# Kernel tuning notes

Hardware: AMD Instinct MI355X
Metric: run time of the kernel (lower is better)

Reference implementation:

```python
import jax, jax.numpy as jnp
import numpy as np
import math

D = 256
NH = 4
MULT = 128
N = MULT * D // NH  # 8192
N_LAYER = 6
VOCAB = 256
THETA = 2 ** 16
EPS = 1e-5


def get_freqs(n):
    ar = jnp.arange(n, dtype=jnp.float32)
    q = jnp.floor(ar / 2.0) * 2.0  # quantize in pairs
    return 1.0 / (THETA ** (q / n)) / (2.0 * math.pi)


def layer_norm(x):
    m = jnp.mean(x, axis=-1, keepdims=True)
    v = jnp.var(x, axis=-1, keepdims=True)
    return (x - m) / jnp.sqrt(v + EPS)


def rope_apply(v, cos, sin):
    # interleaved rotation: v_rot = stack((-v[odd], v[even])) interleaved back
    v_rot = jnp.stack([-v[..., 1::2], v[..., ::2]], axis=-1).reshape(v.shape)
    return v * cos + v_rot * sin


def setup_inputs() -> dict:
    key = jax.random.key(0)
    ks = jax.random.split(key, 6)
    idx = jax.random.randint(ks[0], (1, 1024), 0, VOCAB)
    embed = jax.random.normal(ks[1], (VOCAB, D), dtype=jnp.float32) * 0.02
    encoder = jax.random.normal(ks[2], (NH, D, N), dtype=jnp.float32) * 0.02
    encoder_v = jax.random.normal(ks[3], (NH, D, N), dtype=jnp.float32) * 0.02
    decoder = jax.random.normal(ks[4], (NH * N, D), dtype=jnp.float32) * 0.02
    lm_head = jax.random.normal(ks[5], (D, VOCAB), dtype=jnp.float32) * 0.02
    return {"idx": idx, "embed": embed, "encoder": encoder,
            "encoder_v": encoder_v, "decoder": decoder, "lm_head": lm_head}


def reference(idx, embed, encoder, encoder_v, decoder, lm_head):
    B, T = idx.shape
    x = layer_norm(embed[idx])  # (B, T, D)

    freqs = get_freqs(N)  # (N,)
    phases = (jnp.arange(T, dtype=jnp.float32)[:, None] * freqs[None, :]) % 1.0
    phases = phases * (2.0 * math.pi)
    cos = jnp.cos(phases)[None, None]  # (1,1,T,N)
    sin = jnp.sin(phases)[None, None]

    causal = jnp.tril(jnp.ones((T, T), dtype=jnp.float32), k=-1)  # strict lower

    for _ in range(N_LAYER):
        # x_sparse: (B, nh, T, N)
        x_sparse = jax.nn.relu(jnp.einsum('btd,hdn->bhtn', x, encoder))
        QR = rope_apply(x_sparse, cos, sin)
        # raw (no-softmax) strictly-causal attention, V = x broadcast over heads
        scores = jnp.einsum('bhtn,bhsn->bhts', QR, QR) * causal
        yKV = layer_norm(jnp.einsum('bhts,bsd->bhtd', scores, x))
        y_sparse = jax.nn.relu(jnp.einsum('bhtd,hdn->bhtn', yKV, encoder_v))
        xy = x_sparse * y_sparse  # (B, nh, T, N)
        # head-major flatten then project back to D
        yMLP = xy.transpose(0, 2, 1, 3).reshape(B, T, NH * N) @ decoder
        y = layer_norm(yMLP)
        x = layer_norm(x + y)

    logits = x @ lm_head  # (B, T, VOCAB)
    return logits
```

## Files before the change

### kernel.cpp

```cpp
#include <hip/hip_runtime.h>
#include <math.h>


typedef __bf16 bf16;
typedef bf16  bf16x8 __attribute__((ext_vector_type(8)));
typedef float f32x4  __attribute__((ext_vector_type(4)));

#define BM 128
#define BN 128
#define BK 32
#define SW 32

typedef __attribute__((address_space(3))) unsigned int lds_uint;
typedef const __attribute__((address_space(1))) unsigned int glb_uint;

__device__ __forceinline__ void ld_g2l16(const void* g, void* l) {
  __builtin_amdgcn_global_load_lds((glb_uint*)g, (lds_uint*)l, 16, 0, 0);
}

__device__ __forceinline__ float block_sum256(float v) {
  __shared__ float sb[4];
#pragma unroll
  for (int o = 32; o > 0; o >>= 1) v += __shfl_down(v, o);
  __syncthreads();
  if ((threadIdx.x & 63) == 0) sb[threadIdx.x >> 6] = v;
  __syncthreads();
  return sb[0] + sb[1] + sb[2] + sb[3];
}

template <int MODE>
__global__ __launch_bounds__(256) void gemm_bt(
    const bf16* __restrict__ A, long lda, long aZ, long aZ2,
    const bf16* __restrict__ Bt, long ldb, long bZ, long bZ2,
    void* __restrict__ Cv, long ldc, long cZ,
    void* __restrict__ Dv, long dZ,
    int M, int N, int K) {
  int m0, n0;
  long z = blockIdx.z;
  if (MODE == 6) {
    const int combo = blockIdx.x;
    const int tile  = blockIdx.y;
    const int tr = (int)((sqrtf(8.f * tile + 1.f) - 1.f) * 0.5f);
    const int tc = tile - tr * (tr + 1) / 2;
    m0 = tr * BM; n0 = tc * BN;
    A  += (long)(combo >> 3) * aZ2 + (long)(combo & 7) * aZ;
    Bt += (long)(combo >> 3) * bZ2 + (long)(combo & 7) * bZ;
  } else if (MODE == 7) {
    const int combo = blockIdx.x;
    z = combo;
    m0 = (blockIdx.y >> 1) * BM;
    n0 = (blockIdx.y & 1) * BN;
    A  += (combo & 7) * aZ + (combo >> 3) * aZ2;
    Bt += (combo & 7) * bZ + (combo >> 3) * bZ2;
  } else {
    m0 = blockIdx.y * BM;
    n0 = blockIdx.x * BN;
    if (MODE == 2 && n0 > m0) return;
    A  += (z & 3) * aZ + (z >> 2) * aZ2;
    Bt += (z & 3) * bZ + (z >> 2) * bZ2;
  }

  int kbeg = 0;
  int Keff = K;
  if (MODE == 3) {
    const int s = (int)(z & 3);
    kbeg = s * 256;
    const int kc = m0 + BM;
    Keff = (kbeg + 256 < kc) ? kbeg + 256 : kc;
    if (kbeg >= Keff) return;
  }

  __shared__ __align__(16) bf16 As[3][BM * SW];
  __shared__ __align__(16) bf16 Bs[3][BN * SW];

  const int tid  = threadIdx.x;
  const int lane = tid & 63;
  const int wr   = (tid >> 6) >> 1;
  const int wc   = (tid >> 6) & 1;
  const int l15  = lane & 15;
  const int qd   = lane >> 4;
  const int rj   = qd ^ ((l15 >> 1) & 3);

  f32x4 acc[4][4] = {};

  const int srow = tid >> 2;
  const int skc  = (((tid & 3) ^ ((tid >> 3) & 3))) * 8;
  const bf16* ap = A + (long)(m0 + srow) * lda + skc;
  const bf16* bp = Bt + (long)(n0 + srow) * ldb + skc;

  auto stage = [&](int buf, int k0) {
    char* AsB = (char*)&As[buf][0];
    char* BsB = (char*)&Bs[buf][0];
    ld_g2l16(ap + k0,            AsB + tid * 16);
    ld_g2l16(ap + k0 + 64 * lda, AsB + 4096 + tid * 16);
    ld_g2l16(bp + k0,            BsB + tid * 16);
    ld_g2l16(bp + k0 + 64 * ldb, BsB + 4096 + tid * 16);
  };
  auto compute = [&](int buf) {
    bf16x8 af[4], bfr[4];
#pragma unroll
    for (int i = 0; i < 4; i++)
      af[i] = *(const bf16x8*)&As[buf][(wr * 64 + i * 16 + l15) * SW + rj * 8];
#pragma unroll
    for (int j = 0; j < 4; j++)
      bfr[j] = *(const bf16x8*)&Bs[buf][(wc * 64 + j * 16 + l15) * SW + rj * 8];
    __builtin_amdgcn_s_setprio(1);
#pragma unroll
    for (int i = 0; i < 4; i++)
#pragma unroll
      for (int j = 0; j < 4; j++)
        acc[i][j] = __builtin_amdgcn_mfma_f32_16x16x32_bf16(af[i], bfr[j], acc[i][j], 0, 0, 0);
    __builtin_amdgcn_s_setprio(0);
  };

  const int nst = (Keff - kbeg) >> 5;
  stage(0, kbeg);
  stage(1, kbeg + BK);
  int bc = 0;
  for (int k = 0; k < nst - 1; k++) {
    asm volatile("s_waitcnt vmcnt(4)" ::: "memory");
    __builtin_amdgcn_s_barrier();
    const int k2 = k + 2;
    if (k2 < nst) {
      int b2 = bc + 2; if (b2 >= 3) b2 -= 3;
      stage(b2, kbeg + k2 * BK);
    }
    compute(bc);
    bc = (bc + 1 == 3) ? 0 : bc + 1;
  }
  asm volatile("s_waitcnt vmcnt(0)" ::: "memory");
  __builtin_amdgcn_s_barrier();
  compute(bc);

#pragma unroll
  for (int i = 0; i < 4; i++) {
#pragma unroll
    for (int j = 0; j < 4; j++) {
#pragma unroll
      for (int r = 0; r < 4; r++) {
        const int row = m0 + wr * 64 + i * 16 + qd * 4 + r;
        const int col = n0 + wc * 64 + j * 16 + l15;
        float v = acc[i][j][r];
        if (MODE == 1) {
          float rv = fmaxf(v, 0.f);
          float pv = __shfl_xor(rv, 1);
          ((bf16*)Cv)[z * cZ + (long)row * ldc + col] = (bf16)rv;
          float freq = exp2f(-(float)(col >> 1) * (1.0f / 256.0f)) * 0.15915494309189535f;
          float ph = (float)row * freq;
          ph -= floorf(ph);
          float s, c;
          __sincosf(ph * 6.283185307179586f, &s, &c);
          float rot = (col & 1) ? pv : -pv;
          ((bf16*)Dv)[z * dZ + (long)row * ldc + col] = (bf16)(rv * c + rot * s);
        } else if (MODE == 2) {
          ((bf16*)Cv)[z * cZ + (long)row * ldc + col] = (bf16)((col < row) ? v : 0.f);
        } else if (MODE == 4) {
          float rv = fmaxf(v, 0.f);
          float xv = (float)((const bf16*)Dv)[z * dZ + (long)row * 8192 + col];
          ((bf16*)Cv)[z * cZ + (long)row * ldc + col] = (bf16)(rv * xv);
        } else if (MODE == 6) {
          const int combo = blockIdx.x;
          long base = (((long)(combo & 7) * 4 + (combo >> 3)) * 36 + blockIdx.y) * 16384;
          ((bf16*)Cv)[base + (long)(row - m0) * 128 + (col - n0)] = (bf16)v;
        } else if (MODE == 7) {
          ((bf16*)Cv)[z * cZ + (long)row * ldc + col] = (bf16)v;
        } else {
          ((float*)Cv)[z * cZ + (long)row * ldc + col] = v;
        }
      }
    }
  }
}

__global__ void reduce_sc(const bf16* __restrict__ scpart, bf16* __restrict__ sc) {
  const int tile = blockIdx.x >> 2, q = blockIdx.x & 3, head = blockIdx.y;
  const int tr = (int)((sqrtf(8.f * tile + 1.f) - 1.f) * 0.5f);
  const int tc = tile - tr * (tr + 1) / 2;
  const long t0 = (long)head * 589824 + (long)tile * 16384;
  for (int g = q * 512 + threadIdx.x; g < q * 512 + 512; g += 256) {
    const int i = g * 8;
    float s[8] = {};
#pragma unroll
    for (int sl = 0; sl < 8; sl++) {
      bf16x8 v = *(const bf16x8*)&scpart[(long)sl * 2359296 + t0 + i];
#pragma unroll
      for (int e = 0; e < 8; e++) s[e] += (float)v[e];
    }
    const int lr = i >> 7, lc = i & 127;
    const int grow = tr * 128 + lr, gcol = tc * 128 + lc;
    bf16x8 o;
#pragma unroll
    for (int e = 0; e < 8; e++) o[e] = (bf16)((gcol + e < grow) ? s[e] : 0.f);
    *(bf16x8*)&sc[(long)head * 1048576 + (long)grow * 1024 + gcol] = o;
  }
}

__global__ void transpose_cvt(const float* __restrict__ in, bf16* __restrict__ out,
                              int R, int C, long inZ, long outZ) {
  in += (long)blockIdx.z * inZ;
  out += (long)blockIdx.z * outZ;
  __shared__ float tile[32][33];
  int c0 = blockIdx.x * 32, r0 = blockIdx.y * 32;
  int lc = threadIdx.x & 31, lr8 = threadIdx.x >> 5;
#pragma unroll
  for (int i = 0; i < 32; i += 8)
    tile[lr8 + i][lc] = in[(long)(r0 + lr8 + i) * C + c0 + lc];
  __syncthreads();
#pragma unroll
  for (int i = 0; i < 32; i += 8)
    out[(long)(c0 + lr8 + i) * R + r0 + lc] = (bf16)tile[lc][lr8 + i];
}

__global__ void embed_ln(const int* __restrict__ idx, const float* __restrict__ embed,
                         float* __restrict__ x, bf16* __restrict__ xb,
                         bf16* __restrict__ xT) {
  int t = blockIdx.x, d = threadIdx.x;
  float v = embed[(long)idx[t] * 256 + d];
  float m = block_sum256(v) * (1.0f / 256.0f);
  float c = v - m;
  float var = block_sum256(c * c) * (1.0f / 256.0f);
  float o = c * rsqrtf(var + 1e-5f);
  x[t * 256 + d] = o;
  xb[t * 256 + d] = (bf16)o;
  xT[d * 1024 + t] = (bf16)o;
}

__global__ void ln_rows(const float* __restrict__ ykvp, bf16* __restrict__ out) {
  int r = blockIdx.x, d = threadIdx.x;
  int h = r >> 10, t = r & 1023;
  int ns = (t >> 8) + 1;
  float v = 0.f;
  for (int s = 0; s < ns; s++)
    v += ykvp[((long)(h * 4 + s)) * 262144 + (long)t * 256 + d];
  float m = block_sum256(v) * (1.0f / 256.0f);
  float c = v - m;
  float var = block_sum256(c * c) * (1.0f / 256.0f);
  out[(long)r * 256 + d] = (bf16)(c * rsqrtf(var + 1e-5f));
}

__global__ void ln_fuse(const bf16* __restrict__ part, float* __restrict__ x,
                        bf16* __restrict__ xb, bf16* __restrict__ xT) {
  int t = blockIdx.x, d = threadIdx.x;
  float s = 0.f;
#pragma unroll
  for (int i = 0; i < 32; i++) s += (float)part[(long)i * 262144 + t * 256 + d];
  float m = block_sum256(s) * (1.0f / 256.0f);
  float c = s - m;
  float var = block_sum256(c * c) * (1.0f / 256.0f);
  float y = c * rsqrtf(var + 1e-5f);
  float zv = x[t * 256 + d] + y;
  m = block_sum256(zv) * (1.0f / 256.0f);
  c = zv - m;
  var = block_sum256(c * c) * (1.0f / 256.0f);
  float o = c * rsqrtf(var + 1e-5f);
  x[t * 256 + d] = o;
  xb[t * 256 + d] = (bf16)o;
  xT[d * 1024 + t] = (bf16)o;
}

extern "C" void kernel_launch(void* const* d_in, const int* in_sizes, int n_in,
                              void* d_out, int out_size, void* d_ws, size_t ws_size,
                              hipStream_t stream) {
  const int*   idx = (const int*)d_in[0];
  const float* emb = (const float*)d_in[1];
  float* out = (float*)d_out;
  char* ws  = (char*)d_ws;

  bf16*  encT   = (bf16*)(ws + 0L);
  bf16*  encvT  = (bf16*)(ws + 16777216L);
  bf16*  decT   = (bf16*)(ws + 33554432L);
  bf16*  lmT    = (bf16*)(ws + 50331648L);
  float* x      = (float*)(ws + 50462720L);
  bf16*  xb     = (bf16*)(ws + 51511296L);
  bf16*  xT     = (bf16*)(ws + 52035584L);
  bf16*  xs     = (bf16*)(ws + 52559872L);
  bf16*  qr     = (bf16*)(ws + 119668736L);
  bf16*  sc     = (bf16*)(ws + 186777600L);
  bf16*  scpart = (bf16*)(ws + 195166208L);
  float* ykvp   = (float*)(ws + 195166208L);
  bf16*  part   = (bf16*)(ws + 195166208L);
  bf16*  ykvln  = (bf16*)(ws + 211943424L);
  const bool big = ws_size >= 232914944UL;

  transpose_cvt<<<dim3(256, 8, 4), dim3(256), 0, stream>>>((const float*)d_in[2], encT, 256, 8192, 2097152L, 2097152L);
  transpose_cvt<<<dim3(256, 8, 4), dim3(256), 0, stream>>>((const float*)d_in[3], encvT, 256, 8192, 2097152L, 2097152L);
  transpose_cvt<<<dim3(8, 1024, 1), dim3(256), 0, stream>>>((const float*)d_in[4], decT, 32768, 256, 0L, 0L);
  transpose_cvt<<<dim3(8, 8, 1), dim3(256), 0, stream>>>((const float*)d_in[5], lmT, 256, 256, 0L, 0L);
  embed_ln<<<dim3(1024), dim3(256), 0, stream>>>(idx, emb, x, xb, xT);

  for (int l = 0; l < 6; l++) {
    gemm_bt<1><<<dim3(64, 8, 4), dim3(256), 0, stream>>>(
        xb, 256L, 0L, 0L, encT, 256L, 2097152L, 8388608L,
        (void*)xs, 8192L, 8388608L, (void*)qr, 8388608L, 1024, 8192, 256);
    if (big) {
      gemm_bt<6><<<dim3(32, 36), dim3(256), 0, stream>>>(
          qr, 8192L, 1024L, 8388608L, qr, 8192L, 1024L, 8388608L,
          (void*)scpart, 0L, 0L, (void*)0, 0L, 1024, 1024, 1024);
      reduce_sc<<<dim3(144, 4), dim3(256), 0, stream>>>(scpart, sc);
    } else {
      gemm_bt<2><<<dim3(8, 8, 4), dim3(256), 0, stream>>>(
          qr, 8192L, 8388608L, 33554432L, qr, 8192L, 8388608L, 33554432L,
          (void*)sc, 1024L, 1048576L, (void*)0, 0L, 1024, 1024, 8192);
    }
    gemm_bt<3><<<dim3(2, 8, 16), dim3(256), 0, stream>>>(
        sc, 1024L, 0L, 1048576L, xT, 1024L, 0L, 0L,
        (void*)ykvp, 256L, 262144L, (void*)0, 0L, 1024, 256, 1024);
    ln_rows<<<dim3(4096), dim3(256), 0, stream>>>(ykvp, ykvln);
    gemm_bt<4><<<dim3(64, 8, 4), dim3(256), 0, stream>>>(
        ykvln, 256L, 262144L, 1048576L, encvT, 256L, 2097152L, 8388608L,
        (void*)qr, 8192L, 8388608L, (void*)xs, 8388608L, 1024, 8192, 256);
    gemm_bt<7><<<dim3(32, 16), dim3(256), 0, stream>>>(
        qr, 8192L, 1024L, 8388608L, decT, 32768L, 1024L, 8192L,
        (void*)part, 256L, 262144L, (void*)0, 0L, 1024, 256, 1024);
    ln_fuse<<<dim3(1024), dim3(256), 0, stream>>>(part, x, xb, xT);
  }
  gemm_bt<5><<<dim3(2, 8, 1), dim3(256), 0, stream>>>(
      xb, 256L, 0L, 0L, lmT, 256L, 0L, 0L,
      (void*)out, 256L, 0L, (void*)0, 0L, 1024, 256, 256);
}
```

Measured before the change: 1.309 ms.

## Drop x_sparse store by inverting RoPE in gemm4; add 256x256 causal score GEMM kernel

The encoder GEMM epilogue now writes only the RoPE-rotated activations. The encoder_v GEMM epilogue recovers x_sparse from them by applying the inverse rotation, which removes one large bf16 store per layer. The split-K score GEMM is replaced by a dedicated 512-thread kernel with 256x256 tiles over the lower-triangular tile set. Each workgroup then reuses its loaded operands across more output and launches fewer tiles. The cost is extra sincos work and a lane shuffle in the MODE 4 epilogue, a double bf16 rounding of x_sparse, and some wasted compute on upper-triangle subtiles inside diagonal 256 tiles.

```diff
diff --git a/kernel.cpp b/kernel.cpp
--- a/kernel.cpp
+++ b/kernel.cpp
@@ -37,15 +37,7 @@
     int M, int N, int K) {
   int m0, n0;
   long z = blockIdx.z;
-  if (MODE == 6) {
-    const int combo = blockIdx.x;
-    const int tile  = blockIdx.y;
-    const int tr = (int)((sqrtf(8.f * tile + 1.f) - 1.f) * 0.5f);
-    const int tc = tile - tr * (tr + 1) / 2;
-    m0 = tr * BM; n0 = tc * BN;
-    A  += (long)(combo >> 3) * aZ2 + (long)(combo & 7) * aZ;
-    Bt += (long)(combo >> 3) * bZ2 + (long)(combo & 7) * bZ;
-  } else if (MODE == 7) {
+  if (MODE == 7) {
     const int combo = blockIdx.x;
     z = combo;
     m0 = (blockIdx.y >> 1) * BM;
@@ -144,29 +136,125 @@
         if (MODE == 1) {
           float rv = fmaxf(v, 0.f);
           float pv = __shfl_xor(rv, 1);
-          ((bf16*)Cv)[z * cZ + (long)row * ldc + col] = (bf16)rv;
           float freq = exp2f(-(float)(col >> 1) * (1.0f / 256.0f)) * 0.15915494309189535f;
           float ph = (float)row * freq;
           ph -= floorf(ph);
           float s, c;
           __sincosf(ph * 6.283185307179586f, &s, &c);
           float rot = (col & 1) ? pv : -pv;
-          ((bf16*)Dv)[z * dZ + (long)row * ldc + col] = (bf16)(rv * c + rot * s);
+          ((bf16*)Cv)[z * cZ + (long)row * ldc + col] = (bf16)(rv * c + rot * s);
         } else if (MODE == 2) {
           ((bf16*)Cv)[z * cZ + (long)row * ldc + col] = (bf16)((col < row) ? v : 0.f);
         } else if (MODE == 4) {
           float rv = fmaxf(v, 0.f);
-          float xv = (float)((const bf16*)Dv)[z * dZ + (long)row * 8192 + col];
+          float qv = (float)((const bf16*)Dv)[z * dZ + (long)row * 8192 + col];
+          float pqv = __shfl_xor(qv, 1);
+          float freq = exp2f(-(float)(col >> 1) * (1.0f / 256.0f)) * 0.15915494309189535f;
+          float ph = (float)row * freq;
+          ph -= floorf(ph);
+          float s, c;
+          __sincosf(ph * 6.283185307179586f, &s, &c);
+          float rot = (col & 1) ? -pqv : pqv;
+          float xv = qv * c + rot * s;
           ((bf16*)Cv)[z * cZ + (long)row * ldc + col] = (bf16)(rv * xv);
-        } else if (MODE == 6) {
-          const int combo = blockIdx.x;
-          long base = (((long)(combo & 7) * 4 + (combo >> 3)) * 36 + blockIdx.y) * 16384;
-          ((bf16*)Cv)[base + (long)(row - m0) * 128 + (col - n0)] = (bf16)v;
         } else if (MODE == 7) {
           ((bf16*)Cv)[z * cZ + (long)row * ldc + col] = (bf16)v;
         } else {
           ((float*)Cv)[z * cZ + (long)row * ldc + col] = v;
         }
+      }
+    }
+  }
+}
+
+__global__ __launch_bounds__(512) void gemm_sc256(
+    const bf16* __restrict__ QR, bf16* __restrict__ scpart) {
+  const int wgid  = blockIdx.x;
+  const int slice = wgid & 7;
+  const int j     = wgid >> 3;
+  const int head  = j / 10;
+  const int tile  = j - head * 10;
+  const int tr = (int)((sqrtf(8.f * tile + 1.f) - 1.f) * 0.5f);
+  const int tc = tile - tr * (tr + 1) / 2;
+  const int m0 = tr * 256, n0 = tc * 256;
+  const bf16* Ab = QR + (long)head * 8388608 + (long)slice * 1024;
+
+  __shared__ __align__(16) bf16 As[3][256 * SW];
+  __shared__ __align__(16) bf16 Bs[3][256 * SW];
+
+  const int tid  = threadIdx.x;
+  const int lane = tid & 63;
+  const int w    = tid >> 6;
+  const int wr   = w >> 2;
+  const int wc   = w & 3;
+  const int l15  = lane & 15;
+  const int qd   = lane >> 4;
+  const int rj   = qd ^ ((l15 >> 1) & 3);
+
+  f32x4 acc[8][4] = {};
+
+  const int srow = tid >> 2;
+  const int skc  = (((tid & 3) ^ ((tid >> 3) & 3))) * 8;
+  const bf16* ap = Ab + (long)(m0 + srow) * 8192 + skc;
+  const bf16* bp = Ab + (long)(n0 + srow) * 8192 + skc;
+
+  auto stage = [&](int buf, int k0) {
+    char* AsB = (char*)&As[buf][0];
+    char* BsB = (char*)&Bs[buf][0];
+    ld_g2l16(ap + k0,               AsB + tid * 16);
+    ld_g2l16(ap + k0 + 128L * 8192, AsB + 8192 + tid * 16);
+    ld_g2l16(bp + k0,               BsB + tid * 16);
+    ld_g2l16(bp + k0 + 128L * 8192, BsB + 8192 + tid * 16);
+  };
+  auto compute = [&](int buf) {
+    bf16x8 af[8], bfr[4];
+#pragma unroll
+    for (int i = 0; i < 8; i++)
+      af[i] = *(const bf16x8*)&As[buf][(wr * 128 + i * 16 + l15) * SW + rj * 8];
+#pragma unroll
+    for (int jj = 0; jj < 4; jj++)
+      bfr[jj] = *(const bf16x8*)&Bs[buf][(wc * 64 + jj * 16 + l15) * SW + rj * 8];
+    __builtin_amdgcn_s_setprio(1);
+#pragma unroll
+    for (int i = 0; i < 8; i++)
+#pragma unroll
+      for (int jj = 0; jj < 4; jj++)
+        acc[i][jj] = __builtin_amdgcn_mfma_f32_16x16x32_bf16(af[i], bfr[jj], acc[i][jj], 0, 0, 0);
+    __builtin_amdgcn_s_setprio(0);
+  };
+
+  const int nst = 32;
+  stage(0, 0);
+  stage(1, BK);
+  int bc = 0;
+  for (int k = 0; k < nst - 1; k++) {
+    asm volatile("s_waitcnt vmcnt(4)" ::: "memory");
+    __builtin_amdgcn_s_barrier();
+    const int k2 = k + 2;
+    if (k2 < nst) {
+      int b2 = bc + 2; if (b2 >= 3) b2 -= 3;
+      stage(b2, k2 * BK);
+    }
+    compute(bc);
+    bc = (bc + 1 == 3) ? 0 : bc + 1;
+  }
+  asm volatile("s_waitcnt vmcnt(0)" ::: "memory");
+  __builtin_amdgcn_s_barrier();
+  compute(bc);
+
+  const int R = tr * 2 + wr;
+  const int C = tc * 2 + (wc >> 1);
+  if (R < C) return;
+  bf16* outp = scpart + (((long)slice * 4 + head) * 36 + (long)R * (R + 1) / 2 + C) * 16384;
+#pragma unroll
+  for (int i = 0; i < 8; i++) {
+#pragma unroll
+    for (int jj = 0; jj < 4; jj++) {
+#pragma unroll
+      for (int r = 0; r < 4; r++) {
+        const int lr = i * 16 + qd * 4 + r;
+        const int lc = (wc & 1) * 64 + jj * 16 + l15;
+        outp[(long)lr * 128 + lc] = (bf16)acc[i][jj][r];
       }
     }
   }
@@ -273,7 +361,7 @@
   float* x      = (float*)(ws + 50462720L);
   bf16*  xb     = (bf16*)(ws + 51511296L);
   bf16*  xT     = (bf16*)(ws + 52035584L);
-  bf16*  xs     = (bf16*)(ws + 52559872L);
+  bf16*  xy     = (bf16*)(ws + 52559872L);
   bf16*  qr     = (bf16*)(ws + 119668736L);
   bf16*  sc     = (bf16*)(ws + 186777600L);
   bf16*  scpart = (bf16*)(ws + 195166208L);
@@ -291,11 +379,9 @@
   for (int l = 0; l < 6; l++) {
     gemm_bt<1><<<dim3(64, 8, 4), dim3(256), 0, stream>>>(
         xb, 256L, 0L, 0L, encT, 256L, 2097152L, 8388608L,
-        (void*)xs, 8192L, 8388608L, (void*)qr, 8388608L, 1024, 8192, 256);
+        (void*)qr, 8192L, 8388608L, (void*)0, 0L, 1024, 8192, 256);
     if (big) {
-      gemm_bt<6><<<dim3(32, 36), dim3(256), 0, stream>>>(
-          qr, 8192L, 1024L, 8388608L, qr, 8192L, 1024L, 8388608L,
-          (void*)scpart, 0L, 0L, (void*)0, 0L, 1024, 1024, 1024);
+      gemm_sc256<<<dim3(320), dim3(512), 0, stream>>>(qr, scpart);
       reduce_sc<<<dim3(144, 4), dim3(256), 0, stream>>>(scpart, sc);
     } else {
       gemm_bt<2><<<dim3(8, 8, 4), dim3(256), 0, stream>>>(
@@ -308,9 +394,9 @@
     ln_rows<<<dim3(4096), dim3(256), 0, stream>>>(ykvp, ykvln);
     gemm_bt<4><<<dim3(64, 8, 4), dim3(256), 0, stream>>>(
         ykvln, 256L, 262144L, 1048576L, encvT, 256L, 2097152L, 8388608L,
-        (void*)qr, 8192L, 8388608L, (void*)xs, 8388608L, 1024, 8192, 256);
+        (void*)xy, 8192L, 8388608L, (void*)qr, 8388608L, 1024, 8192, 256);
     gemm_bt<7><<<dim3(32, 16), dim3(256), 0, stream>>>(
-        qr, 8192L, 1024L, 8388608L, decT, 32768L, 1024L, 8192L,
+        xy, 8192L, 1024L, 8388608L, decT, 32768L, 1024L, 8192L,
         (void*)part, 256L, 262144L, (void*)0, 0L, 1024, 256, 1024);
     ln_fuse<<<dim3(1024), dim3(256), 0, stream>>>(part, x, xb, xT);
   }
```

Measured after the change: 1.383 ms. 1.06x slower.
